# Performance work log

Hardware: AMD Instinct MI355X
Metric: run time of the kernel (lower is better)

Reference implementation:

```python
import jax, jax.numpy as jnp
import numpy as np

B, L, D = 2, 2048, 1536
H = 12            # num_heads == num_key_value_heads
FDIM = 16         # feature_dim (per-head q/k dim)
HD = D // H       # head_dim = 128 (per-head v dim)
EPS = 1e-12
W_STD = 0.02


def setup_inputs() -> dict:
    key = jax.random.key(0)
    k0, k1, k2, k3, k4 = jax.random.split(key, 5)
    hidden_states = jax.random.normal(k0, (B, L, D), dtype=jnp.float32)
    Wq = jax.random.normal(k1, (D, H * FDIM), dtype=jnp.float32) * W_STD
    Wk = jax.random.normal(k2, (D, H * FDIM), dtype=jnp.float32) * W_STD
    Wv = jax.random.normal(k3, (D, H * HD), dtype=jnp.float32) * W_STD
    Wo = jax.random.normal(k4, (H * HD, D), dtype=jnp.float32) * W_STD
    return {"hidden_states": hidden_states, "Wq": Wq, "Wk": Wk, "Wv": Wv, "Wo": Wo}


def _split_heads(x, h):
    b, l, hd = x.shape
    return x.reshape(b, l, h, hd // h).transpose(0, 2, 1, 3)  # b h l d


def reference(hidden_states, Wq, Wk, Wv, Wo):
    b, l, _ = hidden_states.shape
    q = _split_heads(hidden_states @ Wq, H)  # [b,h,l,FDIM]
    k = _split_heads(hidden_states @ Wk, H)  # [b,h,l,FDIM]
    v = _split_heads(hidden_states @ Wv, H)  # [b,h,l,HD]

    # parallel_based(q, k, v, eps, use_scale=True, use_normalize=True)
    q = q * (FDIM ** -0.5)
    s = jnp.einsum('bhld,bhmd->bhlm', q, k)            # raw qk scores
    attn = 1.0 + s + 0.5 * s * s                        # 2nd-order Taylor of exp
    causal = jnp.tril(jnp.ones((l, l), dtype=bool))
    attn = jnp.where(causal, attn, 0.0)
    o = jnp.einsum('bhlm,bhmd->bhld', attn, v)          # [b,h,l,HD]
    z = attn.sum(axis=-1)                               # causal normalizer [b,h,l]
    o = o / (z[..., None] + EPS)

    o = o.transpose(0, 2, 1, 3).reshape(b, l, H * HD)   # b l (h d)
    return o @ Wo
```

## Files before the change

### kernel.cpp

```cpp
#include <hip/hip_runtime.h>
#include <hip/hip_bf16.h>

typedef short short8 __attribute__((ext_vector_type(8)));
typedef float f32x4  __attribute__((ext_vector_type(4)));
typedef float f32x16 __attribute__((ext_vector_type(16)));
typedef unsigned int u32x4 __attribute__((ext_vector_type(4)));
typedef unsigned short u16x4 __attribute__((ext_vector_type(4)));

union V16   { u32x4 v; short8 s; };
union U16x8 { u32x4 v; unsigned short u[8]; };
union FB4   { u32x4 v; float f[4]; };
union BF2U  { __hip_bfloat162 h; unsigned int u; };

__device__ inline unsigned short f2bf(float f) {
  union { float f; unsigned int u; } x; x.f = f;
  unsigned int u = x.u + 0x7fffu + ((x.u >> 16) & 1u);
  return (unsigned short)(u >> 16);
}

__device__ __forceinline__ unsigned int pkbf(float a, float b) {
  BF2U p; p.h = __float22bfloat162_rn(make_float2(a, b)); return p.u;
}

__device__ __forceinline__ void plswap(unsigned int& a, unsigned int& b) {
  asm("v_permlane32_swap_b32 %0, %1" : "+v"(a), "+v"(b));
}

__device__ __forceinline__ int probe_fp32(const unsigned short* hs) {
  int bad = 0;
#pragma unroll
  for (int i = 0; i < 64; ++i) {
    unsigned int e = (hs[2 * i] >> 7) & 0xFFu;
    if (e >= 0xFEu || (e > 0u && e < 0x60u)) bad++;
  }
  return bad >= 6;
}

__device__ __forceinline__ void gl_lds16(const unsigned short* g, unsigned short* l) {
  __builtin_amdgcn_global_load_lds(
      (const __attribute__((address_space(1))) unsigned int*)g,
      (__attribute__((address_space(3))) unsigned int*)l, 16, 0, 0);
}

__global__ __launch_bounds__(256) void w_tr(const void* __restrict__ Wq,
                                            const void* __restrict__ Wk,
                                            const void* __restrict__ Wv,
                                            const void* __restrict__ Wo,
                                            const void* __restrict__ hs,
                                            unsigned short* __restrict__ WT,
                                            unsigned short* __restrict__ WoT,
                                            unsigned short* __restrict__ hsb) {
  __shared__ unsigned short t[64 * 72];
  __shared__ int sf;
  const int z = blockIdx.z;
  if (z == 4) {
    if (threadIdx.x == 0) sf = probe_fp32((const unsigned short*)hs);
    __syncthreads();
    const int f = sf;
    size_t i0 = ((size_t)(blockIdx.y * 24 + blockIdx.x) * 256 + threadIdx.x) * 8;
    if (f) {
      const float* in = (const float*)hs;
      FB4 a, b; a.v = *(const u32x4*)&in[i0]; b.v = *(const u32x4*)&in[i0 + 4];
      U16x8 p;
#pragma unroll
      for (int j = 0; j < 4; ++j) { p.u[j] = f2bf(a.f[j]); p.u[j + 4] = f2bf(b.f[j]); }
      *(u32x4*)&hsb[i0] = p.v;
    } else {
      *(u32x4*)&hsb[i0] = *(const u32x4*)((const unsigned short*)hs + i0);
    }
    return;
  }
  if (blockIdx.y >= 24) return;
  const void* in_; unsigned short* out; int C;
  if      (z == 0) { in_ = Wq; out = WT;              C = 192;  }
  else if (z == 1) { in_ = Wk; out = WT + 192 * 1536; C = 192;  }
  else if (z == 2) { in_ = Wv; out = WT + 384 * 1536; C = 1536; }
  else             { in_ = Wo; out = WoT;             C = 1536; }
  const int c0 = blockIdx.x * 64;
  if (c0 >= C) return;
  if (threadIdx.x == 0) sf = probe_fp32((const unsigned short*)hs);
  __syncthreads();
  const int f = sf;
  const int r0 = blockIdx.y * 64;
  const int tx = threadIdx.x & 15;
  const int ty = threadIdx.x >> 4;
#pragma unroll
  for (int j = 0; j < 4; ++j) {
    const int r = ty + 16 * j;
    const size_t idx = (size_t)(r0 + r) * C + c0 + tx * 4;
    float v[4];
    if (f) {
      FB4 a; a.v = *(const u32x4*)&((const float*)in_)[idx];
#pragma unroll
      for (int i = 0; i < 4; ++i) {
        const int c = tx * 4 + i;
        t[c * 72 + (r ^ (((c >> 1) & 7) << 3))] = f2bf(a.f[i]);
      }
    } else {
      u16x4 a = *(const u16x4*)&((const unsigned short*)in_)[idx];
#pragma unroll
      for (int i = 0; i < 4; ++i) {
        const int c = tx * 4 + i;
        t[c * 72 + (r ^ (((c >> 1) & 7) << 3))] = a[i];
      }
    }
  }
  __syncthreads();
#pragma unroll
  for (int jj = 0; jj < 2; ++jj) {
    const int c = (threadIdx.x >> 3) + 32 * jj;
    const int rb = (threadIdx.x & 7) * 8;
    const int rsw = rb ^ (((c >> 1) & 7) << 3);
    u32x4 v = *(const u32x4*)&t[c * 72 + rsw];
    *(u32x4*)&out[(size_t)(c0 + c) * 1536 + r0 + rb] = v;
  }
}

__global__ __launch_bounds__(256) void gemm_bt(const unsigned short* __restrict__ A,
                                               const unsigned short* __restrict__ BT,
                                               void* __restrict__ C_,
                                               int M, int NB, int K, int ldC,
                                               unsigned short* __restrict__ vTout,
                                               const unsigned short* __restrict__ probe_src) {
  __shared__ unsigned short smem[4 * 128 * 64];
#define AS(buf, r, c) smem[(((buf) * 128) + (r)) * 64 + (c)]
#define BS(buf, r, c) smem[(((2 + (buf)) * 128) + (r)) * 64 + (c)]
  const int m0 = blockIdx.y * 128, n0 = blockIdx.x * 128;
  const int tid = threadIdx.x;
  const int lane = tid & 63, w = tid >> 6;
  const int wr = w >> 1, wc = w & 1;
  const int quad = lane >> 4, mrow = lane & 15;

  const int sr = lane >> 3;
  const int sc = ((lane & 7) ^ (lane >> 3)) * 8;
  const int fsw = (mrow & 7);

  const f32x4 zf = {0.f, 0.f, 0.f, 0.f};
  f32x4 acc[4][4];
#pragma unroll
  for (int mt = 0; mt < 4; ++mt)
#pragma unroll
    for (int nt = 0; nt < 4; ++nt) acc[mt][nt] = zf;

  const int nk = K >> 6;
#pragma unroll
  for (int j = 0; j < 4; ++j) {
    const int r = 32 * w + 8 * j + sr;
    gl_lds16(&A [(size_t)(m0 + r) * K + sc], &AS(0, 32 * w + 8 * j, 0));
    gl_lds16(&BT[(size_t)(n0 + r) * K + sc], &BS(0, 32 * w + 8 * j, 0));
  }

  for (int ks = 0; ks < nk; ++ks) {
    const int cur = ks & 1;
    __syncthreads();
    if (ks + 1 < nk) {
      const int k1 = (ks + 1) << 6;
#pragma unroll
      for (int j = 0; j < 4; ++j) {
        const int r = 32 * w + 8 * j + sr;
        gl_lds16(&A [(size_t)(m0 + r) * K + k1 + sc], &AS(cur ^ 1, 32 * w + 8 * j, 0));
        gl_lds16(&BT[(size_t)(n0 + r) * K + k1 + sc], &BS(cur ^ 1, 32 * w + 8 * j, 0));
      }
    }
#pragma unroll
    for (int kq = 0; kq < 2; ++kq) {
      short8 afr[4], bfr[4];
#pragma unroll
      for (int mt = 0; mt < 4; ++mt) {
        V16 u; u.v = *(const u32x4*)&AS(cur, wr * 64 + mt * 16 + mrow, ((kq * 4 + quad) ^ fsw) * 8);
        afr[mt] = u.s;
      }
#pragma unroll
      for (int nt = 0; nt < 4; ++nt) {
        V16 u; u.v = *(const u32x4*)&BS(cur, wc * 64 + nt * 16 + mrow, ((kq * 4 + quad) ^ fsw) * 8);
        bfr[nt] = u.s;
      }
#pragma unroll
      for (int mt = 0; mt < 4; ++mt)
#pragma unroll
        for (int nt = 0; nt < 4; ++nt)
          acc[mt][nt] = __builtin_amdgcn_mfma_f32_16x16x32_bf16(afr[mt], bfr[nt], acc[mt][nt], 0, 0, 0);
    }
  }

  __syncthreads();
  if (vTout != nullptr && n0 >= 384) {
    unsigned short* T = smem + w * (64 * 72);
#pragma unroll
    for (int mt = 0; mt < 4; ++mt)
#pragma unroll
      for (int nt = 0; nt < 4; ++nt)
#pragma unroll
        for (int r = 0; r < 4; ++r)
          T[(nt * 16 + mrow) * 72 + mt * 16 + quad * 4 + r] = f2bf(acc[mt][nt][r]);
    asm volatile("s_waitcnt lgkmcnt(0)" ::: "memory");
    const int h  = (n0 - 384) >> 7;
    const int gb = (m0 + wr * 64) >> 11;
    const int l0 = (m0 + wr * 64) & 2047;
    const size_t vrow0 = ((size_t)(gb * 12 + h) << 7) + wc * 64;
#pragma unroll
    for (int i = 0; i < 8; ++i) {
      const int row = (lane >> 3) + 8 * i;
      const int ch  = (lane & 7) * 8;
      u32x4 vv = *(const u32x4*)&T[row * 72 + ch];
      *(u32x4*)&vTout[(vrow0 + row) * 2048 + l0 + ch] = vv;
    }
  } else {
    const int of = probe_src ? probe_fp32(probe_src) : 0;
#pragma unroll
    for (int mt = 0; mt < 4; ++mt)
#pragma unroll
      for (int nt = 0; nt < 4; ++nt)
#pragma unroll
        for (int r = 0; r < 4; ++r) {
          int grow = m0 + wr * 64 + mt * 16 + quad * 4 + r;
          int gcol = n0 + wc * 64 + nt * 16 + mrow;
          size_t idx = (size_t)grow * ldC + gcol;
          if (of) ((float*)C_)[idx] = acc[mt][nt][r];
          else    ((unsigned short*)C_)[idx] = f2bf(acc[mt][nt][r]);
        }
  }
#undef AS
#undef BS
}

__global__ __launch_bounds__(256, 3) void attn_based(const unsigned short* __restrict__ qkv,
                                                     const unsigned short* __restrict__ vT,
                                                     unsigned short* __restrict__ obuf) {
  __shared__ unsigned short Vs[2][128][64];
  __shared__ float zbuf[2][32];
  const int LD = 384;
  const int bh = blockIdx.x;
  const int qt = 31 - blockIdx.y;
  const int b = bh / 12, h = bh % 12;
  const int tid = threadIdx.x;
  const int lane = tid & 63, w = tid >> 6;
  const int qsub = w & 1, kvp = w >> 1;
  const int col = lane & 31, hi = lane >> 5;

  const int q0 = qt * 64 + qsub * 32;
  const int q_abs = q0 + col;

  V16 bq; bq.v = *(const u32x4*)&qkv[(size_t)(b * 2048 + q_abs) * LD + h * 16 + hi * 8];

  const unsigned short* kptr =
      &qkv[(size_t)(b * 2048 + kvp * 32 + col) * LD + 192 + h * 16 + hi * 8];

  const unsigned short* vbase = vT + (size_t)(bh * 128) * 2048;

  const f32x16 z16 = {0.f,0.f,0.f,0.f,0.f,0.f,0.f,0.f,0.f,0.f,0.f,0.f,0.f,0.f,0.f,0.f};
  f32x16 oacc[4];
#pragma unroll
  for (int nc = 0; nc < 4; ++nc) oacc[nc] = z16;
  float zcA[4] = {0.f, 0.f, 0.f, 0.f};

#define STAGE_V(KV0, BUF)                                                     \
  {                                                                           \
    _Pragma("unroll")                                                         \
    for (int j = 0; j < 4; ++j) {                                             \
      const int row = 32 * w + 8 * j + (lane >> 3);                           \
      gl_lds16(vbase + (size_t)row * 2048 + (KV0) + ((lane & 7) ^ (lane >> 3)) * 8, \
               &Vs[BUF][32 * w + 8 * j][0]);                                  \
    }                                                                         \
  }

  STAGE_V(0, 0);
  V16 kf; kf.v = *(const u32x4*)kptr;
  __syncthreads();

  for (int t = 0; t <= qt; ++t) {
    const int cur = t & 1;
    if (t < qt) STAGE_V((t + 1) * 64, cur ^ 1);

    V16 kfn;
    kptr += (size_t)64 * LD;
    if (t < qt) kfn.v = *(const u32x4*)kptr;

    const bool live = (t < qt) | (kvp <= qsub);
    if (live) {
      f32x16 st = __builtin_amdgcn_mfma_f32_32x32x16_bf16(kf.s, bq.s, z16, 0, 0, 0);
      const int kv0 = t * 64 + kvp * 32;
      const bool diag = (t == qt) & (kvp == qsub);
      float pr[16];
      if (diag) {
#pragma unroll
        for (int r = 0; r < 16; ++r) {
          float s = st[r];
          float a = fmaf(s, fmaf(s, 0.03125f, 0.25f), 1.0f);
          const int kvr = kv0 + (r & 3) + 8 * (r >> 2) + 4 * hi;
          a = (kvr <= q_abs) ? a : 0.0f;
          zcA[r & 3] += a; pr[r] = a;
        }
      } else {
#pragma unroll
        for (int r = 0; r < 16; ++r) {
          float s = st[r];
          float a = fmaf(s, fmaf(s, 0.03125f, 0.25f), 1.0f);
          zcA[r & 3] += a; pr[r] = a;
        }
      }

      union PA { short8 s; unsigned int wd[4]; } pa0, pa1;
      {
        unsigned int x0 = pkbf(pr[0], pr[1]), x1 = pkbf(pr[2], pr[3]);
        unsigned int y0 = pkbf(pr[4], pr[5]), y1 = pkbf(pr[6], pr[7]);
        plswap(x0, y0); plswap(x1, y1);
        pa0.wd[0] = x0; pa0.wd[1] = x1; pa0.wd[2] = y0; pa0.wd[3] = y1;
      }
      {
        unsigned int x0 = pkbf(pr[8], pr[9]),  x1 = pkbf(pr[10], pr[11]);
        unsigned int y0 = pkbf(pr[12], pr[13]), y1 = pkbf(pr[14], pr[15]);
        plswap(x0, y0); plswap(x1, y1);
        pa1.wd[0] = x0; pa1.wd[1] = x1; pa1.wd[2] = y0; pa1.wd[3] = y1;
      }

      __builtin_amdgcn_s_setprio(1);
#pragma unroll
      for (int nc = 0; nc < 4; ++nc) {
        const int hd = nc * 32 + col;
        V16 v0, v1;
        v0.v = *(const u32x4*)&Vs[cur][hd][(((kvp * 4 + hi)     ^ (hd & 7)) * 8)];
        v1.v = *(const u32x4*)&Vs[cur][hd][(((kvp * 4 + 2 + hi) ^ (hd & 7)) * 8)];
        oacc[nc] = __builtin_amdgcn_mfma_f32_32x32x16_bf16(pa0.s, v0.s, oacc[nc], 0, 0, 0);
        oacc[nc] = __builtin_amdgcn_mfma_f32_32x32x16_bf16(pa1.s, v1.s, oacc[nc], 0, 0, 0);
      }
      __builtin_amdgcn_s_setprio(0);
    }
    __syncthreads();
    if (t < qt) kf = kfn;
  }

  float zcol = (zcA[0] + zcA[1]) + (zcA[2] + zcA[3]);
  zcol += __shfl_xor(zcol, 32, 64);

  float* fbuf = (float*)&Vs[0][0][0];
  if (w >= 2) {
    const int base = (w & 1) * 4096;
#pragma unroll
    for (int nc = 0; nc < 4; ++nc)
#pragma unroll
      for (int g = 0; g < 4; ++g) {
        f32x4 v = {oacc[nc][4 * g], oacc[nc][4 * g + 1],
                   oacc[nc][4 * g + 2], oacc[nc][4 * g + 3]};
        *(f32x4*)&fbuf[base + ((nc * 4 + g) * 64 + lane) * 4] = v;
      }
    if (lane < 32) zbuf[w & 1][lane] = zcol;
  }
  __syncthreads();
  if (w < 2) {
    const int base = w * 4096;
#pragma unroll
    for (int nc = 0; nc < 4; ++nc)
#pragma unroll
      for (int g = 0; g < 4; ++g) {
        f32x4 v = *(const f32x4*)&fbuf[base + ((nc * 4 + g) * 64 + lane) * 4];
#pragma unroll
        for (int r = 0; r < 4; ++r) oacc[nc][4 * g + r] += v[r];
      }
    const float zinv = 1.0f / (zcol + zbuf[w][col] + 1e-12f);
#pragma unroll
    for (int g = 0; g < 4; ++g)
#pragma unroll
      for (int rr = 0; rr < 4; ++rr) {
        const int qrow = rr + 8 * g + 4 * hi;
        const float iv = __shfl(zinv, qrow, 64);
        const size_t base_o = (size_t)(b * 2048 + q0 + qrow) * 1536 + h * 128 + col;
#pragma unroll
        for (int nc = 0; nc < 4; ++nc)
          obuf[base_o + nc * 32] = f2bf(oacc[nc][4 * g + rr] * iv);
      }
  }
#undef STAGE_V
}

extern "C" void kernel_launch(void* const* d_in, const int* in_sizes, int n_in,
                              void* d_out, int out_size, void* d_ws, size_t ws_size,
                              hipStream_t stream) {
  const void* hs = d_in[0];
  const void* Wq = d_in[1];
  const void* Wk = d_in[2];
  const void* Wv = d_in[3];
  const void* Wo = d_in[4];
  const unsigned short* hsp = (const unsigned short*)hs;

  unsigned short* ws   = (unsigned short*)d_ws;
  unsigned short* WT   = ws;
  unsigned short* WoT  = WT + 1920 * 1536;
  unsigned short* qkvb = WoT + 1536 * 1536;
  unsigned short* hsb  = qkvb + 4096 * 384;
  unsigned short* vT   = hsb + 4096 * 1536;
  unsigned short* obuf = hsb;

  w_tr<<<dim3(24, 128, 5), 256, 0, stream>>>(Wq, Wk, Wv, Wo, hs, WT, WoT, hsb);

  gemm_bt<<<dim3(15, 32, 1), 256, 0, stream>>>(hsb, WT, qkvb, 4096, 1920, 1536,
                                               384, vT, nullptr);

  attn_based<<<dim3(24, 32, 1), 256, 0, stream>>>(qkvb, vT, obuf);

  gemm_bt<<<dim3(12, 32, 1), 256, 0, stream>>>(obuf, WoT, d_out, 4096, 1536, 1536,
                                               1536, nullptr, hsp);
}
```

Baseline: 199.6 us.

## Triple-buffer V staging with counted vmcnt waits and XCD-aware GEMM tile remap

The attention kernel moves from double to triple buffering of the V tile in LDS and prefetches two tiles ahead. It replaces __syncthreads with explicit s_waitcnt vmcnt counts plus a raw s_barrier, fenced by sched_barrier, so the next loads can stay in flight across the barrier. The GEMM also remaps block IDs so consecutive tiles land on the same XCD, which should improve L2 reuse. The risks are more LDS per block (lower occupancy at 3 blocks per CU) and fragile hand-counted vmcnt values.

```diff
diff --git a/kernel.cpp b/kernel.cpp
--- a/kernel.cpp
+++ b/kernel.cpp
@@ -41,6 +41,8 @@
       (const __attribute__((address_space(1))) unsigned int*)g,
       (__attribute__((address_space(3))) unsigned int*)l, 16, 0, 0);
 }
+
+#define PIN() __builtin_amdgcn_sched_barrier(0)
 
 __global__ __launch_bounds__(256) void w_tr(const void* __restrict__ Wq,
                                             const void* __restrict__ Wk,
@@ -88,7 +90,6 @@
   for (int j = 0; j < 4; ++j) {
     const int r = ty + 16 * j;
     const size_t idx = (size_t)(r0 + r) * C + c0 + tx * 4;
-    float v[4];
     if (f) {
       FB4 a; a.v = *(const u32x4*)&((const float*)in_)[idx];
 #pragma unroll
@@ -125,7 +126,13 @@
   __shared__ unsigned short smem[4 * 128 * 64];
 #define AS(buf, r, c) smem[(((buf) * 128) + (r)) * 64 + (c)]
 #define BS(buf, r, c) smem[(((2 + (buf)) * 128) + (r)) * 64 + (c)]
-  const int m0 = blockIdx.y * 128, n0 = blockIdx.x * 128;
+  const int gx = gridDim.x;
+  const int nwg = gx * gridDim.y;
+  const int orig = blockIdx.y * gx + blockIdx.x;
+  const int q8 = nwg >> 3, r8 = nwg & 7;
+  const int xcd = orig & 7, inner = orig >> 3;
+  const int wg = (xcd < r8 ? xcd * (q8 + 1) : r8 * (q8 + 1) + (xcd - r8) * q8) + inner;
+  const int m0 = (wg / gx) * 128, n0 = (wg % gx) * 128;
   const int tid = threadIdx.x;
   const int lane = tid & 63, w = tid >> 6;
   const int wr = w >> 1, wc = w & 1;
@@ -227,7 +234,7 @@
 __global__ __launch_bounds__(256, 3) void attn_based(const unsigned short* __restrict__ qkv,
                                                      const unsigned short* __restrict__ vT,
                                                      unsigned short* __restrict__ obuf) {
-  __shared__ unsigned short Vs[2][128][64];
+  __shared__ unsigned short Vs[3][128][64];
   __shared__ float zbuf[2][32];
   const int LD = 384;
   const int bh = blockIdx.x;
@@ -266,15 +273,27 @@
 
   STAGE_V(0, 0);
   V16 kf; kf.v = *(const u32x4*)kptr;
-  __syncthreads();
+  PIN();
+  if (qt >= 1) {
+    STAGE_V(64, 1);
+    asm volatile("s_waitcnt vmcnt(4)" ::: "memory");
+  } else {
+    asm volatile("s_waitcnt vmcnt(0)" ::: "memory");
+  }
+  PIN();
+  __builtin_amdgcn_s_barrier();
+  PIN();
 
   for (int t = 0; t <= qt; ++t) {
-    const int cur = t & 1;
-    if (t < qt) STAGE_V((t + 1) * 64, cur ^ 1);
+    const int cur = t % 3;
 
     V16 kfn;
-    kptr += (size_t)64 * LD;
-    if (t < qt) kfn.v = *(const u32x4*)kptr;
+    if (t < qt) {
+      kptr += (size_t)64 * LD;
+      kfn.v = *(const u32x4*)kptr;
+    }
+    PIN();
+    if (t + 2 <= qt) STAGE_V((t + 2) * 64, (t + 2) % 3);
 
     const bool live = (t < qt) | (kvp <= qsub);
     if (live) {
@@ -326,7 +345,14 @@
       }
       __builtin_amdgcn_s_setprio(0);
     }
-    __syncthreads();
+    if (t + 2 <= qt) {
+      asm volatile("s_waitcnt vmcnt(4)" ::: "memory");
+    } else {
+      asm volatile("s_waitcnt vmcnt(0)" ::: "memory");
+    }
+    PIN();
+    __builtin_amdgcn_s_barrier();
+    PIN();
     if (t < qt) kf = kfn;
   }
 
```

After: 193.7 us. 2.9% less time.
